# Optimization experiments

Hardware: AMD Instinct MI355X
Metric: run time of the kernel (lower is better)

## Reference

```python
import jax, jax.numpy as jnp
import numpy as np

EPS = 1e-08
RMAX = 8.0          # hist_range_max
BINS = 256
ALPHA = 0.02        # kalman_alpha (EMA rate)
THRESH = -2.0       # mask_threshold


def setup_inputs() -> dict:
    key = jax.random.key(0)
    B, C, L = 4, 5, 2097152
    x = jax.random.normal(key, (B, C, L), dtype=jnp.float32)
    # running histogram buffer, initialized to ones as in the module
    hist = jnp.ones((C, BINS), dtype=jnp.float32)
    # analytic reference log-pdfs over the bin grid
    grid = jnp.linspace(EPS, RMAX, BINS)
    logp_ref = jnp.stack([
        jnp.log(grid) - 0.5 * grid ** 2,                 # Rayleigh-like (A)
        -1.5 * jnp.log1p((grid / (RMAX / 2)) ** 2),      # heavy-tail (theta')
        -grid,                                            # exponential (A^2)
        -0.5 * grid ** 2,                                 # half-gaussian (AA')
        -0.5 * grid ** 2,                                 # half-gaussian (A^2 theta')
    ], axis=0) + EPS
    return {"x": x, "hist": hist, "logp_ref": logp_ref.astype(jnp.float32)}


def reference(x, hist, logp_ref):
    B, C, L = x.shape
    # NOTE: torch does x.reshape(C, -1) on a (B, C, L) tensor, i.e. a raw
    # memory reinterpretation (no permute). Replicate exactly.
    flat_abs = jnp.abs(x.reshape(C, B * L))                     # (C, B*L)
    # per-channel 99th-percentile normalization (linear interpolation, like torch)
    max_vals = jnp.maximum(
        jnp.quantile(flat_abs, 0.99, axis=-1, keepdims=True), EPS)
    normalized = flat_abs / max_vals * RMAX
    clipped = jnp.clip(normalized, 0.0, RMAX - EPS)
    idx = (clipped / RMAX * (BINS - 1)).astype(jnp.int32)       # floor (nonneg)
    idx = jnp.clip(idx, 0, BINS - 1)                            # (C, B*L)

    # histogram scatter-add per channel (vectorized over all channels)
    ch = jnp.broadcast_to(jnp.arange(C)[:, None], idx.shape)
    new_hist = jnp.zeros((C, BINS), dtype=x.dtype).at[ch, idx].add(1.0)

    # EMA update of the running histogram
    hist = (1.0 - ALPHA) * hist + ALPHA * new_hist
    smoothed = hist + EPS
    logp_obs = jnp.log(smoothed / jnp.sum(smoothed, axis=-1, keepdims=True))

    # gather per-sample log-probs and form the log-likelihood ratio
    logp_ref_s = jnp.take_along_axis(logp_ref, idx, axis=-1)   # (C, B*L)
    logp_obs_s = jnp.take_along_axis(logp_obs, idx, axis=-1)   # (C, B*L)
    Lam = (logp_ref_s - logp_obs_s).reshape(B, C, L)

    mask = jax.nn.sigmoid(-(Lam - THRESH))   # beta = 1.0
    return x * mask
```

## Files before the change

kernel.cpp:

```cpp
#include <hip/hip_runtime.h>
#include <math.h>

typedef unsigned int u32;
typedef unsigned long long u64;
typedef long long i64;
typedef float float4n __attribute__((ext_vector_type(4)));

#define BINS 256
#define TBITS 0x40000000u
#define A_BASE 131072u
#define A_BINS 4096
#define B_BINS 8192
#define SLOT 1152
#define NBLK 512


__device__ __forceinline__ int bin_index_f32(float xv, float mv) {
    float r = __fdiv_rn(fabsf(xv), mv);
    r = fminf(r, 1.0f);
    return (int)__fmul_rn(r, 255.0f);
}

template<int PER>
__device__ void block_select(const u32* __restrict__ h, u32 target,
                             u32* ssum, u32* res) {
    const int t = threadIdx.x;
    u32 loc[PER];
    u32 s = 0;
    const int base = t * PER;
#pragma unroll
    for (int j = 0; j < PER; ++j) { loc[j] = h[base + j]; s += loc[j]; }
    ssum[t] = s;
    __syncthreads();
    for (int off = 1; off < 256; off <<= 1) {
        u32 add = (t >= off) ? ssum[t - off] : 0;
        __syncthreads();
        ssum[t] += add;
        __syncthreads();
    }
    u32 cum = ssum[t] - s;
#pragma unroll
    for (int j = 0; j < PER; ++j) {
        u32 cnt = loc[j];
        if (target >= cum && target < cum + cnt) { res[0] = (u32)(base + j); res[1] = target - cum; }
        cum += cnt;
    }
    __syncthreads();
}

__device__ __forceinline__ float np_lerp_f32(u32 v0bits, u32 v1bits, double gamma) {
    float v0 = __uint_as_float(v0bits);
    float v1 = __uint_as_float(v1bits);
    float dba = __fsub_rn(v1, v0);
    float q;
    if (gamma >= 0.5) q = __fsub_rn(v1, __fmul_rn(dba, (float)(1.0 - gamma)));
    else              q = __fadd_rn(v0, __fmul_rn(dba, (float)gamma));
    return fmaxf(q, 1e-8f);
}


__global__ __launch_bounds__(256) void k_pass1(const float* __restrict__ x, u32* __restrict__ cand,
                                               u32* __restrict__ gha, u32* __restrict__ oflow,
                                               u32* __restrict__ goob, i64 nper, int do_cand) {
    __shared__ u32 lbuf[SLOT];
    __shared__ u32 lha[A_BINS];
    __shared__ u32 lcnt, loob;
    const int c = blockIdx.y;
    for (int i = threadIdx.x; i < A_BINS; i += 256) lha[i] = 0;
    if (threadIdx.x == 0) { lcnt = 0; loob = 0; }
    __syncthreads();
    const float* xc = x + (i64)c * nper;
    const i64 nv = nper >> 2;
    const float4* xv = (const float4*)xc;
    for (i64 i = (i64)blockIdx.x * 256 + threadIdx.x; i < nv; i += (i64)gridDim.x * 256) {
        float4 v = xv[i];
        u32 b;
        b = __float_as_uint(fabsf(v.x));
        if (b >= TBITS) { u32 p = atomicAdd(&lcnt, 1u); if (p < SLOT) lbuf[p] = b;
                          u32 bin = (b >> 13) - A_BASE; if (bin >= A_BINS) { atomicAdd(&loob, 1u); bin = A_BINS - 1; }
                          atomicAdd(&lha[bin], 1u); }
        b = __float_as_uint(fabsf(v.y));
        if (b >= TBITS) { u32 p = atomicAdd(&lcnt, 1u); if (p < SLOT) lbuf[p] = b;
                          u32 bin = (b >> 13) - A_BASE; if (bin >= A_BINS) { atomicAdd(&loob, 1u); bin = A_BINS - 1; }
                          atomicAdd(&lha[bin], 1u); }
        b = __float_as_uint(fabsf(v.z));
        if (b >= TBITS) { u32 p = atomicAdd(&lcnt, 1u); if (p < SLOT) lbuf[p] = b;
                          u32 bin = (b >> 13) - A_BASE; if (bin >= A_BINS) { atomicAdd(&loob, 1u); bin = A_BINS - 1; }
                          atomicAdd(&lha[bin], 1u); }
        b = __float_as_uint(fabsf(v.w));
        if (b >= TBITS) { u32 p = atomicAdd(&lcnt, 1u); if (p < SLOT) lbuf[p] = b;
                          u32 bin = (b >> 13) - A_BASE; if (bin >= A_BINS) { atomicAdd(&loob, 1u); bin = A_BINS - 1; }
                          atomicAdd(&lha[bin], 1u); }
    }
    if (blockIdx.x == 0 && threadIdx.x < (int)(nper & 3)) {
        u32 b = __float_as_uint(fabsf(xc[nv * 4 + threadIdx.x]));
        if (b >= TBITS) { u32 p = atomicAdd(&lcnt, 1u); if (p < SLOT) lbuf[p] = b;
                          u32 bin = (b >> 13) - A_BASE; if (bin >= A_BINS) { atomicAdd(&loob, 1u); bin = A_BINS - 1; }
                          atomicAdd(&lha[bin], 1u); }
    }
    __syncthreads();
    for (int i = threadIdx.x; i < A_BINS; i += 256)
        if (lha[i]) atomicAdd(&gha[c * A_BINS + i], lha[i]);
    if (threadIdx.x == 0) {
        if (loob) atomicExch(&goob[c], 1u);
        if (lcnt > SLOT) { atomicExch(&oflow[c], 1u); lcnt = SLOT; }
    }
    __syncthreads();
    if (do_cand) {
        const u32 cnt = lcnt;
        u32* slot = cand + ((i64)c * gridDim.x + blockIdx.x) * SLOT;
        for (u32 j = threadIdx.x; j < SLOT; j += 256)
            slot[j] = (j < cnt) ? lbuf[j] : 0u;
    }
}


__global__ __launch_bounds__(256) void k_cselB_hist(const u32* __restrict__ cand, const u32* __restrict__ gha,
                                                    const u32* __restrict__ oflow, const u32* __restrict__ goob,
                                                    u32* __restrict__ flag, u32* __restrict__ cselA,
                                                    u32* __restrict__ g3a, u32* __restrict__ g3b,
                                                    i64 ntot, u32 needed) {
    __shared__ u32 la[B_BINS], lb[B_BINS];
    __shared__ u32 ssum[256];
    __shared__ u32 prA[4];
    __shared__ u32 s_total;
    const int c = blockIdx.y;
    const int t = threadIdx.x;
    if (t < 4) prA[t] = 0;
    const u32* h = gha + c * A_BINS;
    u32 loc[16];
    u32 s = 0;
    const int base = t * 16;
#pragma unroll
    for (int j = 0; j < 16; ++j) { loc[j] = h[base + j]; s += loc[j]; }
    ssum[t] = s;
    __syncthreads();
    for (int off = 1; off < 256; off <<= 1) {
        u32 add = (t >= off) ? ssum[t - off] : 0;
        __syncthreads();
        ssum[t] += add;
        __syncthreads();
    }
    if (t == 255) s_total = ssum[255];
    __syncthreads();
    const u32 total = s_total;
    const u32 bad = (oflow[c] != 0) || (goob[c] != 0) || (total < needed) || (needed < 2);
    if (bad) {
        if (blockIdx.x == 0 && t == 0) flag[c] = 1u;
        return;
    }
    const u32 t0 = total - needed;
    const u32 t1 = t0 + 1;
    u32 cum = ssum[t] - s;
#pragma unroll
    for (int j = 0; j < 16; ++j) {
        u32 cnt = loc[j];
        if (t0 >= cum && t0 < cum + cnt) { prA[0] = (u32)(base + j); prA[1] = t0 - cum; }
        if (t1 >= cum && t1 < cum + cnt) { prA[2] = (u32)(base + j); prA[3] = t1 - cum; }
        cum += cnt;
    }
    __syncthreads();
    const u32 topA0 = A_BASE + prA[0];
    const u32 topA1 = A_BASE + prA[2];
    if (blockIdx.x == 0 && t == 0) {
        flag[c] = 0u;
        cselA[c * 4 + 0] = prA[0]; cselA[c * 4 + 1] = prA[1];
        cselA[c * 4 + 2] = prA[2]; cselA[c * 4 + 3] = prA[3];
    }
    for (int i = t; i < B_BINS; i += 256) { la[i] = 0; lb[i] = 0; }
    __syncthreads();
    const uint4* cd = (const uint4*)(cand + (i64)c * ntot);
    const i64 nv4 = ntot >> 2;
    for (i64 i = (i64)blockIdx.x * 256 + t; i < nv4; i += (i64)gridDim.x * 256) {
        uint4 v = cd[i];
        u32 b;
        b = v.x;
        if (b >= TBITS) { u32 tb = b >> 13; if (tb == topA0) atomicAdd(&la[b & (B_BINS - 1)], 1u); if (tb == topA1) atomicAdd(&lb[b & (B_BINS - 1)], 1u); }
        b = v.y;
        if (b >= TBITS) { u32 tb = b >> 13; if (tb == topA0) atomicAdd(&la[b & (B_BINS - 1)], 1u); if (tb == topA1) atomicAdd(&lb[b & (B_BINS - 1)], 1u); }
        b = v.z;
        if (b >= TBITS) { u32 tb = b >> 13; if (tb == topA0) atomicAdd(&la[b & (B_BINS - 1)], 1u); if (tb == topA1) atomicAdd(&lb[b & (B_BINS - 1)], 1u); }
        b = v.w;
        if (b >= TBITS) { u32 tb = b >> 13; if (tb == topA0) atomicAdd(&la[b & (B_BINS - 1)], 1u); if (tb == topA1) atomicAdd(&lb[b & (B_BINS - 1)], 1u); }
    }
    __syncthreads();
    for (int i = t; i < B_BINS; i += 256) {
        if (la[i]) atomicAdd(&g3a[c * B_BINS + i], la[i]);
        if (lb[i]) atomicAdd(&g3b[c * B_BINS + i], lb[i]);
    }
}

__global__ void k_flag_force(u32* __restrict__ flag, int C) {
    if (threadIdx.x < C) flag[threadIdx.x] = 1u;
}


__global__ __launch_bounds__(256) void k_mv_final(const float* __restrict__ x, const u32* __restrict__ flag,
                                                  const u32* __restrict__ cselA,
                                                  const u32* __restrict__ g3a, const u32* __restrict__ g3b,
                                                  float* __restrict__ mv, i64 nper, u32 k0, double gamma) {
    __shared__ u32 h0[2048], h1[2048];
    __shared__ u32 ssum[256];
    __shared__ u32 pr[4];
    __shared__ u32 st[4];
    const int c = blockIdx.x;
    const int t = threadIdx.x;

    if (!flag[c]) {
        if (t < 4) pr[t] = 0;
        __syncthreads();
        block_select<32>(g3a + c * B_BINS, cselA[c * 4 + 1], ssum, &pr[0]);
        block_select<32>(g3b + c * B_BINS, cselA[c * 4 + 3], ssum, &pr[2]);
        if (t == 0) {
            u32 v0bits = ((A_BASE + cselA[c * 4 + 0]) << 13) | pr[0];
            u32 v1bits = ((A_BASE + cselA[c * 4 + 2]) << 13) | pr[2];
            mv[c] = np_lerp_f32(v0bits, v1bits, gamma);
        }
        return;
    }

    const float* xc = x + (i64)c * nper;
    const i64 nv = nper >> 2;
    const int rem = (int)(nper & 3);
    const float4* xv = (const float4*)xc;

    for (int i = t; i < 1024; i += 256) h0[i] = 0;
    __syncthreads();
    for (i64 i = t; i < nv; i += 256) {
        float4 v = xv[i];
        atomicAdd(&h0[__float_as_uint(fabsf(v.x)) >> 21], 1u);
        atomicAdd(&h0[__float_as_uint(fabsf(v.y)) >> 21], 1u);
        atomicAdd(&h0[__float_as_uint(fabsf(v.z)) >> 21], 1u);
        atomicAdd(&h0[__float_as_uint(fabsf(v.w)) >> 21], 1u);
    }
    if (t < rem) atomicAdd(&h0[__float_as_uint(fabsf(xc[nv * 4 + t])) >> 21], 1u);
    __syncthreads();
    if (t < 4) pr[t] = 0;
    __syncthreads();
    block_select<4>(h0, k0, ssum, &pr[0]);
    block_select<4>(h0, k0 + 1, ssum, &pr[2]);
    if (t < 4) st[t] = pr[t];
    __syncthreads();

    const u32 p0 = st[0], p1 = st[2];
    for (int i = t; i < 2048; i += 256) { h0[i] = 0; h1[i] = 0; }
    __syncthreads();
    for (i64 i = t; i < nv; i += 256) {
        float4 v = xv[i];
        u32 b;
        b = __float_as_uint(fabsf(v.x));
        if ((b >> 21) == p0) atomicAdd(&h0[(b >> 10) & 2047], 1u);
        if ((b >> 21) == p1) atomicAdd(&h1[(b >> 10) & 2047], 1u);
        b = __float_as_uint(fabsf(v.y));
        if ((b >> 21) == p0) atomicAdd(&h0[(b >> 10) & 2047], 1u);
        if ((b >> 21) == p1) atomicAdd(&h1[(b >> 10) & 2047], 1u);
        b = __float_as_uint(fabsf(v.z));
        if ((b >> 21) == p0) atomicAdd(&h0[(b >> 10) & 2047], 1u);
        if ((b >> 21) == p1) atomicAdd(&h1[(b >> 10) & 2047], 1u);
        b = __float_as_uint(fabsf(v.w));
        if ((b >> 21) == p0) atomicAdd(&h0[(b >> 10) & 2047], 1u);
        if ((b >> 21) == p1) atomicAdd(&h1[(b >> 10) & 2047], 1u);
    }
    if (t < rem) {
        u32 b = __float_as_uint(fabsf(xc[nv * 4 + t]));
        if ((b >> 21) == p0) atomicAdd(&h0[(b >> 10) & 2047], 1u);
        if ((b >> 21) == p1) atomicAdd(&h1[(b >> 10) & 2047], 1u);
    }
    __syncthreads();
    if (t < 4) pr[t] = 0;
    __syncthreads();
    block_select<8>(h0, st[1], ssum, &pr[0]);
    block_select<8>(h1, st[3], ssum, &pr[2]);
    if (t == 0) { st[0] = (p0 << 11) | pr[0]; st[1] = pr[1]; st[2] = (p1 << 11) | pr[2]; st[3] = pr[3]; }
    __syncthreads();

    const u32 q0 = st[0], q1 = st[2];
    for (int i = t; i < 1024; i += 256) { h0[i] = 0; h1[i] = 0; }
    __syncthreads();
    for (i64 i = t; i < nv; i += 256) {
        float4 v = xv[i];
        u32 b;
        b = __float_as_uint(fabsf(v.x));
        if ((b >> 10) == q0) atomicAdd(&h0[b & 1023], 1u);
        if ((b >> 10) == q1) atomicAdd(&h1[b & 1023], 1u);
        b = __float_as_uint(fabsf(v.y));
        if ((b >> 10) == q0) atomicAdd(&h0[b & 1023], 1u);
        if ((b >> 10) == q1) atomicAdd(&h1[b & 1023], 1u);
        b = __float_as_uint(fabsf(v.z));
        if ((b >> 10) == q0) atomicAdd(&h0[b & 1023], 1u);
        if ((b >> 10) == q1) atomicAdd(&h1[b & 1023], 1u);
        b = __float_as_uint(fabsf(v.w));
        if ((b >> 10) == q0) atomicAdd(&h0[b & 1023], 1u);
        if ((b >> 10) == q1) atomicAdd(&h1[b & 1023], 1u);
    }
    if (t < rem) {
        u32 b = __float_as_uint(fabsf(xc[nv * 4 + t]));
        if ((b >> 10) == q0) atomicAdd(&h0[b & 1023], 1u);
        if ((b >> 10) == q1) atomicAdd(&h1[b & 1023], 1u);
    }
    __syncthreads();
    if (t < 4) pr[t] = 0;
    __syncthreads();
    block_select<4>(h0, st[1], ssum, &pr[0]);
    block_select<4>(h1, st[3], ssum, &pr[2]);
    if (t == 0) {
        u32 v0bits = (q0 << 10) | pr[0];
        u32 v1bits = (q1 << 10) | pr[2];
        mv[c] = np_lerp_f32(v0bits, v1bits, gamma);
    }
}


__global__ __launch_bounds__(256) void k_hist_idx(const float* __restrict__ x, const float* __restrict__ mv,
                                                  u32* __restrict__ h256, i64 nper) {
    __shared__ u32 lh[8][257];
    const int c = blockIdx.y;
    const float m = mv[c];
    for (int i = threadIdx.x; i < 8 * 257; i += 256) (&lh[0][0])[i] = 0;
    __syncthreads();
    const float* xc = x + (i64)c * nper;
    const i64 nv = nper >> 2;
    const int copy = threadIdx.x & 7;
    const float4* xv = (const float4*)xc;
    for (i64 i = (i64)blockIdx.x * 256 + threadIdx.x; i < nv; i += (i64)gridDim.x * 256) {
        float4 v = xv[i];
        atomicAdd(&lh[copy][bin_index_f32(v.x, m)], 1u);
        atomicAdd(&lh[copy][bin_index_f32(v.y, m)], 1u);
        atomicAdd(&lh[copy][bin_index_f32(v.z, m)], 1u);
        atomicAdd(&lh[copy][bin_index_f32(v.w, m)], 1u);
    }
    if (blockIdx.x == 0 && threadIdx.x < (int)(nper & 3)) {
        atomicAdd(&lh[copy][bin_index_f32(xc[nv * 4 + threadIdx.x], m)], 1u);
    }
    __syncthreads();
    for (int i = threadIdx.x; i < BINS; i += 256) {
        u32 s = 0;
#pragma unroll
        for (int k = 0; k < 8; ++k) s += lh[k][i];
        if (s) atomicAdd(&h256[c * BINS + i], s);
    }
}


__global__ __launch_bounds__(256) void k_output(const float* __restrict__ x, const float* __restrict__ mv,
                                                const float* __restrict__ hist_in, const float* __restrict__ logp_ref,
                                                const u32* __restrict__ h256, float* __restrict__ out, i64 nper) {
    __shared__ double smv_s[BINS];
    __shared__ double maskl[BINS];
    __shared__ double stot;
    const int c = blockIdx.y;
    const int b = threadIdx.x;
    float h = hist_in[c * BINS + b];
    float nn = (float)h256[c * BINS + b];
    float t = __fadd_rn(__fmul_rn(0.98f, h), __fmul_rn(0.02f, nn));
    float smf = __fadd_rn(t, 1e-8f);
    double sm = (double)smf;
    smv_s[b] = sm;
    __syncthreads();
    if (b < 64) {
        double s = smv_s[b] + smv_s[b + 64] + smv_s[b + 128] + smv_s[b + 192];
        for (int o = 32; o; o >>= 1) s += __shfl_down(s, o);
        if (b == 0) stot = s;
    }
    __syncthreads();
    double Lam = (double)logp_ref[c * BINS + b] - log(sm / stot);
    maskl[b] = 1.0 / (1.0 + exp(Lam + 2.0));
    __syncthreads();

    const float m = mv[c];
    const float* xc = x + (i64)c * nper;
    float* oc = out + (i64)c * nper;
    const i64 nv = nper >> 2;
    const float4* xv = (const float4*)xc;
    float4n* ov = (float4n*)oc;
    for (i64 i = (i64)blockIdx.x * 256 + threadIdx.x; i < nv; i += (i64)gridDim.x * 256) {
        float4 v = xv[i];
        float4n o;
        o.x = (float)((double)v.x * maskl[bin_index_f32(v.x, m)]);
        o.y = (float)((double)v.y * maskl[bin_index_f32(v.y, m)]);
        o.z = (float)((double)v.z * maskl[bin_index_f32(v.z, m)]);
        o.w = (float)((double)v.w * maskl[bin_index_f32(v.w, m)]);
        __builtin_nontemporal_store(o, &ov[i]);
    }
    if (blockIdx.x == 0 && threadIdx.x < (int)(nper & 3)) {
        i64 i = nv * 4 + threadIdx.x;
        float v = xc[i];
        oc[i] = (float)((double)v * maskl[bin_index_f32(v, m)]);
    }
}


extern "C" void kernel_launch(void* const* d_in, const int* in_sizes, int n_in,
                              void* d_out, int out_size, void* d_ws, size_t ws_size,
                              hipStream_t stream) {
    const float* x        = (const float*)d_in[0];
    const float* hist_in  = (const float*)d_in[1];
    const float* logp_ref = (const float*)d_in[2];
    float* out = (float*)d_out;

    const int C = in_sizes[1] / BINS;
    const i64 total = (i64)in_sizes[0];
    const i64 nper = total / C;

    char* w = (char*)d_ws;
    size_t off = 0;
    float* mv   = (float*)(w + off); off += 4 * ((C + 7) & ~7);
    u32* h256   = (u32*)(w + off); off += 4 * BINS * C;
    u32* oflow  = (u32*)(w + off); off += 4 * C;
    u32* goob   = (u32*)(w + off); off += 4 * C;
    u32* flag   = (u32*)(w + off); off += 4 * C;
    u32* cselA  = (u32*)(w + off); off += 4 * 4 * C;
    u32* gha    = (u32*)(w + off); off += 4 * A_BINS * C;
    u32* g3a    = (u32*)(w + off); off += 4 * B_BINS * C;
    u32* g3b    = (u32*)(w + off); off += 4 * B_BINS * C;
    const size_t zbytes = off;
    off = (off + 255) & ~(size_t)255;
    u32* cand = (u32*)(w + off);
    const i64 ntot = (i64)NBLK * SLOT;
    const size_t cand_bytes = (size_t)4 * (size_t)C * (size_t)ntot;
    const int do_cand = (ws_size >= off + cand_bytes) ? 1 : 0;

    (void)hipMemsetAsync(d_ws, 0, zbytes, stream);

    const double virt = 0.99 * (double)(nper - 1);
    const i64 k0 = (i64)floor(virt);
    const double gamma = virt - (double)k0;
    const u32 needed = (u32)(nper - k0);

    dim3 blk(256);
    dim3 grd(NBLK, (unsigned)C);
    dim3 grd64(64, (unsigned)C);

    k_pass1<<<grd, blk, 0, stream>>>(x, cand, gha, oflow, goob, nper, do_cand);
    if (do_cand) {
        k_cselB_hist<<<grd64, blk, 0, stream>>>(cand, gha, oflow, goob, flag, cselA, g3a, g3b, ntot, needed);
    } else {
        k_flag_force<<<1, 64, 0, stream>>>(flag, C);
    }
    k_mv_final<<<(unsigned)C, blk, 0, stream>>>(x, flag, cselA, g3a, g3b, mv, nper, (u32)k0, gamma);
    k_hist_idx<<<grd, blk, 0, stream>>>(x, mv, h256, nper);
    k_output<<<grd, blk, 0, stream>>>(x, mv, hist_in, logp_ref, h256, out, nper);
}
```

Before: 190.5 us.

## Aggregate candidate-append atomics per wavefront, use float mask table, nontemporal candidate I/O

Candidate appends in the first pass now use a wavefront ballot with one leader atomicAdd on the shared counter, replacing one atomic per qualifying element. Candidate slot writes and reads in the select kernel switch to nontemporal stores and loads. The output kernel stores its 256-entry mask table as float rather than double, halving LDS traffic per gather, though the product is still formed in double. This changes the order in which candidates land in the buffer and adds ballot and shuffle overhead on every element, even when no lane qualifies.

```diff
diff --git a/kernel.cpp b/kernel.cpp
--- a/kernel.cpp
+++ b/kernel.cpp
@@ -5,6 +5,7 @@
 typedef unsigned long long u64;
 typedef long long i64;
 typedef float float4n __attribute__((ext_vector_type(4)));
+typedef u32   uint4n  __attribute__((ext_vector_type(4)));
 
 #define BINS 256
 #define TBITS 0x40000000u
@@ -58,6 +59,26 @@
     return fmaxf(q, 1e-8f);
 }
 
+__device__ __forceinline__ void append_cand(u32 b, u32* lbuf, u32* lcnt,
+                                            u32* lha, u32* loob) {
+    const bool pred = (b >= TBITS);
+    u64 m = __ballot(pred);
+    if (m) {
+        const int lane = threadIdx.x & 63;
+        const int leader = __ffsll((unsigned long long)m) - 1;
+        u32 base = 0;
+        if (lane == leader) base = atomicAdd(lcnt, (u32)__popcll(m));
+        base = __shfl(base, leader, 64);
+        if (pred) {
+            u32 p = base + (u32)__popcll(m & ((1ull << lane) - 1ull));
+            if (p < SLOT) lbuf[p] = b;
+            u32 bin = (b >> 13) - A_BASE;
+            if (bin >= A_BINS) { atomicAdd(loob, 1u); bin = A_BINS - 1; }
+            atomicAdd(&lha[bin], 1u);
+        }
+    }
+}
+
 
 __global__ __launch_bounds__(256) void k_pass1(const float* __restrict__ x, u32* __restrict__ cand,
                                                u32* __restrict__ gha, u32* __restrict__ oflow,
@@ -74,29 +95,13 @@
     const float4* xv = (const float4*)xc;
     for (i64 i = (i64)blockIdx.x * 256 + threadIdx.x; i < nv; i += (i64)gridDim.x * 256) {
         float4 v = xv[i];
-        u32 b;
-        b = __float_as_uint(fabsf(v.x));
-        if (b >= TBITS) { u32 p = atomicAdd(&lcnt, 1u); if (p < SLOT) lbuf[p] = b;
-                          u32 bin = (b >> 13) - A_BASE; if (bin >= A_BINS) { atomicAdd(&loob, 1u); bin = A_BINS - 1; }
-                          atomicAdd(&lha[bin], 1u); }
-        b = __float_as_uint(fabsf(v.y));
-        if (b >= TBITS) { u32 p = atomicAdd(&lcnt, 1u); if (p < SLOT) lbuf[p] = b;
-                          u32 bin = (b >> 13) - A_BASE; if (bin >= A_BINS) { atomicAdd(&loob, 1u); bin = A_BINS - 1; }
-                          atomicAdd(&lha[bin], 1u); }
-        b = __float_as_uint(fabsf(v.z));
-        if (b >= TBITS) { u32 p = atomicAdd(&lcnt, 1u); if (p < SLOT) lbuf[p] = b;
-                          u32 bin = (b >> 13) - A_BASE; if (bin >= A_BINS) { atomicAdd(&loob, 1u); bin = A_BINS - 1; }
-                          atomicAdd(&lha[bin], 1u); }
-        b = __float_as_uint(fabsf(v.w));
-        if (b >= TBITS) { u32 p = atomicAdd(&lcnt, 1u); if (p < SLOT) lbuf[p] = b;
-                          u32 bin = (b >> 13) - A_BASE; if (bin >= A_BINS) { atomicAdd(&loob, 1u); bin = A_BINS - 1; }
-                          atomicAdd(&lha[bin], 1u); }
+        append_cand(__float_as_uint(fabsf(v.x)), lbuf, &lcnt, lha, &loob);
+        append_cand(__float_as_uint(fabsf(v.y)), lbuf, &lcnt, lha, &loob);
+        append_cand(__float_as_uint(fabsf(v.z)), lbuf, &lcnt, lha, &loob);
+        append_cand(__float_as_uint(fabsf(v.w)), lbuf, &lcnt, lha, &loob);
     }
     if (blockIdx.x == 0 && threadIdx.x < (int)(nper & 3)) {
-        u32 b = __float_as_uint(fabsf(xc[nv * 4 + threadIdx.x]));
-        if (b >= TBITS) { u32 p = atomicAdd(&lcnt, 1u); if (p < SLOT) lbuf[p] = b;
-                          u32 bin = (b >> 13) - A_BASE; if (bin >= A_BINS) { atomicAdd(&loob, 1u); bin = A_BINS - 1; }
-                          atomicAdd(&lha[bin], 1u); }
+        append_cand(__float_as_uint(fabsf(xc[nv * 4 + threadIdx.x])), lbuf, &lcnt, lha, &loob);
     }
     __syncthreads();
     for (int i = threadIdx.x; i < A_BINS; i += 256)
@@ -109,8 +114,10 @@
     if (do_cand) {
         const u32 cnt = lcnt;
         u32* slot = cand + ((i64)c * gridDim.x + blockIdx.x) * SLOT;
-        for (u32 j = threadIdx.x; j < SLOT; j += 256)
-            slot[j] = (j < cnt) ? lbuf[j] : 0u;
+        for (u32 j = threadIdx.x; j < SLOT; j += 256) {
+            u32 val = (j < cnt) ? lbuf[j] : 0u;
+            __builtin_nontemporal_store(val, &slot[j]);
+        }
     }
 }
 
@@ -169,10 +176,10 @@
     }
     for (int i = t; i < B_BINS; i += 256) { la[i] = 0; lb[i] = 0; }
     __syncthreads();
-    const uint4* cd = (const uint4*)(cand + (i64)c * ntot);
+    const uint4n* cd = (const uint4n*)(cand + (i64)c * ntot);
     const i64 nv4 = ntot >> 2;
     for (i64 i = (i64)blockIdx.x * 256 + t; i < nv4; i += (i64)gridDim.x * 256) {
-        uint4 v = cd[i];
+        uint4n v = __builtin_nontemporal_load(&cd[i]);
         u32 b;
         b = v.x;
         if (b >= TBITS) { u32 tb = b >> 13; if (tb == topA0) atomicAdd(&la[b & (B_BINS - 1)], 1u); if (tb == topA1) atomicAdd(&lb[b & (B_BINS - 1)], 1u); }
@@ -346,7 +353,7 @@
                                                 const float* __restrict__ hist_in, const float* __restrict__ logp_ref,
                                                 const u32* __restrict__ h256, float* __restrict__ out, i64 nper) {
     __shared__ double smv_s[BINS];
-    __shared__ double maskl[BINS];
+    __shared__ float maskl[BINS];
     __shared__ double stot;
     const int c = blockIdx.y;
     const int b = threadIdx.x;
@@ -364,7 +371,7 @@
     }
     __syncthreads();
     double Lam = (double)logp_ref[c * BINS + b] - log(sm / stot);
-    maskl[b] = 1.0 / (1.0 + exp(Lam + 2.0));
+    maskl[b] = (float)(1.0 / (1.0 + exp(Lam + 2.0)));
     __syncthreads();
 
     const float m = mv[c];
@@ -376,16 +383,16 @@
     for (i64 i = (i64)blockIdx.x * 256 + threadIdx.x; i < nv; i += (i64)gridDim.x * 256) {
         float4 v = xv[i];
         float4n o;
-        o.x = (float)((double)v.x * maskl[bin_index_f32(v.x, m)]);
-        o.y = (float)((double)v.y * maskl[bin_index_f32(v.y, m)]);
-        o.z = (float)((double)v.z * maskl[bin_index_f32(v.z, m)]);
-        o.w = (float)((double)v.w * maskl[bin_index_f32(v.w, m)]);
+        o.x = (float)((double)v.x * (double)maskl[bin_index_f32(v.x, m)]);
+        o.y = (float)((double)v.y * (double)maskl[bin_index_f32(v.y, m)]);
+        o.z = (float)((double)v.z * (double)maskl[bin_index_f32(v.z, m)]);
+        o.w = (float)((double)v.w * (double)maskl[bin_index_f32(v.w, m)]);
         __builtin_nontemporal_store(o, &ov[i]);
     }
     if (blockIdx.x == 0 && threadIdx.x < (int)(nper & 3)) {
         i64 i = nv * 4 + threadIdx.x;
         float v = xc[i];
-        oc[i] = (float)((double)v * maskl[bin_index_f32(v, m)]);
+        oc[i] = (float)((double)v * (double)maskl[bin_index_f32(v, m)]);
     }
 }
 
```

Result: slower. 195.0 us (+2.4%).
